# Optimization experiments

Hardware: AMD Instinct MI355X
Metric: run time of the kernel (lower is better)

Reference implementation:

```python
import jax, jax.numpy as jnp
import numpy as np

N, MEM_SIZE, MEM_DIM = 65536, 2048, 256

def setup_inputs() -> dict:
    key = jax.random.key(0)
    k1, k2 = jax.random.split(key)
    x = jax.random.normal(k1, (N, MEM_DIM), dtype=jnp.float32)
    # xavier_uniform for memory parameter [memory_size, memory_dim]
    limit = np.sqrt(6.0 / (MEM_SIZE + MEM_DIM)).astype(np.float32)
    memory = jax.random.uniform(k2, (MEM_SIZE, MEM_DIM), dtype=jnp.float32,
                                minval=-limit, maxval=limit)
    return {"x": x, "memory": memory}

def reference(x, memory):
    # scores: [N, memory_size] = x @ memory^T (unscaled)
    scores = jnp.einsum('nd,md->nm', x, memory)
    attention_weights = jax.nn.softmax(scores, axis=-1)
    memory_output = jnp.einsum('nm,md->nd', attention_weights, memory)
    return (memory_output, attention_weights)
```

## Files before the change

### kernel.cpp

```cpp
#include <hip/hip_runtime.h>
#include <hip/hip_bf16.h>
#include <stdint.h>

#define NQ 65536
#define MM 2048
#define DD 256

typedef __bf16 bf16x8 __attribute__((ext_vector_type(8)));
typedef float f32x16 __attribute__((ext_vector_type(16)));
typedef unsigned short u16;
typedef unsigned int u32;
typedef u16 u16x8 __attribute__((ext_vector_type(8)));

typedef __attribute__((address_space(3))) u32 lds_u32;
typedef __attribute__((address_space(1))) u32 glb_u32;

#define GLOAD16(gsrc, ldst)                                                    \
  __builtin_amdgcn_global_load_lds((glb_u32*)(uintptr_t)(gsrc),                \
                                   (lds_u32*)(u32)(uintptr_t)(ldst), 16, 0, 0)

__device__ __forceinline__ u16 f32_to_bf16_rtne(float v) {
  u32 u = __builtin_bit_cast(u32, v);
  u += 0x7FFFu + ((u >> 16) & 1u);
  return (u16)(u >> 16);
}

__global__ __launch_bounds__(256) void mem_convert_kernel(
    const float* __restrict__ memory, u16* __restrict__ memb,
    u16* __restrict__ memTswz) {
  int tid = blockIdx.x * 256 + threadIdx.x;
  u16 b = f32_to_bf16_rtne(memory[tid]);
  memb[tid] = b;
  int m = tid >> 8, d = tid & 255;
  int t = m >> 5, mi = m & 31;
  int c = mi >> 3, e = mi & 7;
  int slot = c ^ ((d >> 1) & 3);
  memTswz[(size_t)t * 8192 + (size_t)(d * 4 + slot) * 8 + e] = b;
}

__global__ __launch_bounds__(256, 2) void pass1_kernel(
    const float* __restrict__ x, const u16* __restrict__ memb,
    u16* __restrict__ p_e, float* __restrict__ sums) {
  __shared__ __align__(16) char stage[2][32768];

  const int tid = threadIdx.x;
  const int wv = tid >> 6;
  const int l = tid & 63;
  const int q5 = l & 31;
  const int h = l >> 5;
  const int qw = blockIdx.x * 128 + wv * 32;

  bf16x8 aq[16];
  {
    const float* xrow = x + (size_t)(qw + q5) * DD;
#pragma unroll
    for (int ks = 0; ks < 16; ++ks) {
      const float4 f0 = *(const float4*)(xrow + ks * 16 + h * 8);
      const float4 f1 = *(const float4*)(xrow + ks * 16 + h * 8 + 4);
      bf16x8 a;
      a[0] = (__bf16)f0.x; a[1] = (__bf16)f0.y;
      a[2] = (__bf16)f0.z; a[3] = (__bf16)f0.w;
      a[4] = (__bf16)f1.x; a[5] = (__bf16)f1.y;
      a[6] = (__bf16)f1.z; a[7] = (__bf16)f1.w;
      aq[ks] = a;
    }
  }

  auto STAGE1 = [&](int mt, char* buf) {
#pragma unroll
    for (int i = 0; i < 8; ++i) {
      const int wc = wv * 8 + i;
      const int row = wc * 2 + h;
      const int csrc = q5 ^ (row & 7);
      GLOAD16(memb + (((size_t)(mt * 64 + row)) << 8) + csrc * 8,
              buf + (wc << 10));
    }
  };

  float part[16];
#pragma unroll
  for (int r = 0; r < 16; ++r) part[r] = 0.f;

  STAGE1(0, stage[0]);
  __syncthreads();
  for (int mt = 0; mt < 32; ++mt) {
    char* cur = stage[mt & 1];
    char* nxt = stage[(mt & 1) ^ 1];
    if (mt + 1 < 32) STAGE1(mt + 1, nxt);
#pragma unroll
    for (int msub = 0; msub < 2; ++msub) {
      const int mrow = msub * 32 + q5;
      const char* bbase = cur + mrow * 512;
      const int sw = mrow & 7;
      f32x16 acc = 0.f;
      __builtin_amdgcn_s_setprio(1);
#pragma unroll
      for (int ks = 0; ks < 16; ++ks) {
        bf16x8 b = *(const bf16x8*)(bbase + (((ks * 2 + h) ^ sw) << 4));
        acc = __builtin_amdgcn_mfma_f32_32x32x16_bf16(aq[ks], b, acc, 0, 0, 0);
      }
      __builtin_amdgcn_s_setprio(0);
      const int tm = mt * 2 + msub;
#pragma unroll
      for (int r = 0; r < 16; ++r) {
        const int qrow = (r & 3) + 8 * (r >> 2) + 4 * h;
        const float e = __expf(acc[r]);
        part[r] += e;
        p_e[(size_t)(qw + qrow) * MM + tm * 32 + q5] = f32_to_bf16_rtne(e);
      }
    }
    __syncthreads();
  }

#pragma unroll
  for (int r = 0; r < 16; ++r) {
    float p = part[r];
    p += __shfl_xor(p, 1, 64);
    p += __shfl_xor(p, 2, 64);
    p += __shfl_xor(p, 4, 64);
    p += __shfl_xor(p, 8, 64);
    p += __shfl_xor(p, 16, 64);
    if (q5 == 0) sums[qw + (r & 3) + 8 * (r >> 2) + 4 * h] = p;
  }
}

__global__ __launch_bounds__(256, 2) void pass2_kernel(
    const u16* __restrict__ p_e, const u16* __restrict__ memTswz,
    const float* __restrict__ sums, float* __restrict__ outO,
    float* __restrict__ outW) {
  __shared__ __align__(16) char tstage[2][32768];

  const int tid = threadIdx.x;
  const int wv = tid >> 6;
  const int l = tid & 63;
  const int q5 = l & 31;
  const int h = l >> 5;
  const int qw = blockIdx.x * 128 + wv * 32;

  const float inv_lane = 1.0f / sums[qw + q5];
  float invr[16];
#pragma unroll
  for (int r = 0; r < 16; ++r) {
    invr[r] = __shfl(inv_lane, (r & 3) + 8 * (r >> 2) + 4 * h, 64);
  }

  auto STAGE2T = [&](int pr, char* buf) {
#pragma unroll
    for (int i = 0; i < 8; ++i) {
      const int ci = wv * 8 + i;
      GLOAD16(memTswz + ((size_t)pr * 2048 + ci * 64 + l) * 8,
              buf + (ci << 10));
    }
  };

  const u16* prow_base = p_e + (size_t)(qw + q5) * MM;
  u16x8 pec[4], pen[4];
#pragma unroll
  for (int j = 0; j < 4; ++j) {
    pec[j] = *(const u16x8*)(prow_base + (j >> 1) * 32 + (j & 1) * 16 + h * 8);
  }

  f32x16 oacc[8];
#pragma unroll
  for (int i = 0; i < 8; ++i) oacc[i] = 0.f;

  STAGE2T(0, tstage[0]);
  __syncthreads();
  for (int pr = 0; pr < 32; ++pr) {
    char* cur = tstage[pr & 1];
    char* nxt = tstage[(pr & 1) ^ 1];
    if (pr + 1 < 32) {
      STAGE2T(pr + 1, nxt);
      const u16* prow = prow_base + (pr + 1) * 64;
#pragma unroll
      for (int j = 0; j < 4; ++j) {
        pen[j] = *(const u16x8*)(prow + (j >> 1) * 32 + (j & 1) * 16 + h * 8);
      }
    }

#pragma unroll
    for (int tmi = 0; tmi < 2; ++tmi) {
      const char* ct = cur + tmi * 16384;
#pragma unroll
      for (int ks2 = 0; ks2 < 2; ++ks2) {
        const u16x8 pe = pec[tmi * 2 + ks2];
        float w[8];
#pragma unroll
        for (int j = 0; j < 8; ++j) {
          w[j] = __builtin_bit_cast(float, (u32)pe[j] << 16) * inv_lane;
        }
        float* base = outW + (size_t)(qw + q5) * MM + (pr * 2 + tmi) * 32 +
                      ks2 * 16 + h * 8;
        *(float4*)base = make_float4(w[0], w[1], w[2], w[3]);
        *(float4*)(base + 4) = make_float4(w[4], w[5], w[6], w[7]);
      }
      __builtin_amdgcn_s_setprio(1);
#pragma unroll
      for (int ks2 = 0; ks2 < 2; ++ks2) {
        const bf16x8 pa = __builtin_bit_cast(bf16x8, pec[tmi * 2 + ks2]);
#pragma unroll
        for (int dsub = 0; dsub < 8; ++dsub) {
          const int d = dsub * 32 + q5;
          const int slot = (2 * ks2 + h) ^ ((d >> 1) & 3);
          bf16x8 b = *(const bf16x8*)(ct + d * 64 + slot * 16);
          oacc[dsub] = __builtin_amdgcn_mfma_f32_32x32x16_bf16(pa, b,
                                                               oacc[dsub], 0,
                                                               0, 0);
        }
      }
      __builtin_amdgcn_s_setprio(0);
    }
    __syncthreads();
#pragma unroll
    for (int j = 0; j < 4; ++j) pec[j] = pen[j];
  }

#pragma unroll
  for (int dsub = 0; dsub < 8; ++dsub) {
#pragma unroll
    for (int r = 0; r < 16; ++r) {
      const int qrow = (r & 3) + 8 * (r >> 2) + 4 * h;
      outO[(size_t)(qw + qrow) * DD + dsub * 32 + q5] = oacc[dsub][r] * invr[r];
    }
  }
}

__global__ __launch_bounds__(256, 2) void pass1_fb(
    const float* __restrict__ x, const u16* __restrict__ memb,
    float* __restrict__ outWf, float* __restrict__ sums) {
  __shared__ __align__(16) char stage[2][32768];
  const int tid = threadIdx.x;
  const int wv = tid >> 6;
  const int l = tid & 63;
  const int q5 = l & 31;
  const int h = l >> 5;
  const int qw = blockIdx.x * 128 + wv * 32;

  bf16x8 aq[16];
  {
    const float* xrow = x + (size_t)(qw + q5) * DD;
#pragma unroll
    for (int ks = 0; ks < 16; ++ks) {
      const float4 f0 = *(const float4*)(xrow + ks * 16 + h * 8);
      const float4 f1 = *(const float4*)(xrow + ks * 16 + h * 8 + 4);
      bf16x8 a;
      a[0] = (__bf16)f0.x; a[1] = (__bf16)f0.y;
      a[2] = (__bf16)f0.z; a[3] = (__bf16)f0.w;
      a[4] = (__bf16)f1.x; a[5] = (__bf16)f1.y;
      a[6] = (__bf16)f1.z; a[7] = (__bf16)f1.w;
      aq[ks] = a;
    }
  }
  auto STAGE1 = [&](int mt, char* buf) {
#pragma unroll
    for (int i = 0; i < 8; ++i) {
      const int wc = wv * 8 + i;
      const int row = wc * 2 + h;
      const int csrc = q5 ^ (row & 7);
      GLOAD16(memb + (((size_t)(mt * 64 + row)) << 8) + csrc * 8,
              buf + (wc << 10));
    }
  };
  float part[16];
#pragma unroll
  for (int r = 0; r < 16; ++r) part[r] = 0.f;
  STAGE1(0, stage[0]);
  __syncthreads();
  for (int mt = 0; mt < 32; ++mt) {
    char* cur = stage[mt & 1];
    char* nxt = stage[(mt & 1) ^ 1];
    if (mt + 1 < 32) STAGE1(mt + 1, nxt);
#pragma unroll
    for (int msub = 0; msub < 2; ++msub) {
      const int mrow = msub * 32 + q5;
      const char* bbase = cur + mrow * 512;
      const int sw = mrow & 7;
      f32x16 acc = 0.f;
#pragma unroll
      for (int ks = 0; ks < 16; ++ks) {
        bf16x8 b = *(const bf16x8*)(bbase + (((ks * 2 + h) ^ sw) << 4));
        acc = __builtin_amdgcn_mfma_f32_32x32x16_bf16(aq[ks], b, acc, 0, 0, 0);
      }
      const int tm = mt * 2 + msub;
#pragma unroll
      for (int r = 0; r < 16; ++r) {
        const int qrow = (r & 3) + 8 * (r >> 2) + 4 * h;
        const float e = __expf(acc[r]);
        part[r] += e;
        outWf[(size_t)(qw + qrow) * MM + tm * 32 + q5] = e;
      }
    }
    __syncthreads();
  }
#pragma unroll
  for (int r = 0; r < 16; ++r) {
    float s = part[r];
    s += __shfl_xor(s, 1, 64);
    s += __shfl_xor(s, 2, 64);
    s += __shfl_xor(s, 4, 64);
    s += __shfl_xor(s, 8, 64);
    s += __shfl_xor(s, 16, 64);
    if (q5 == 0) sums[qw + (r & 3) + 8 * (r >> 2) + 4 * h] = s;
  }
}

__global__ __launch_bounds__(256, 2) void pass2_fb(
    const u16* __restrict__ memTswz, const float* __restrict__ sums,
    float* __restrict__ outO, float* __restrict__ outW) {
  __shared__ __align__(16) char tstage[2][16384];
  const int tid = threadIdx.x;
  const int wv = tid >> 6;
  const int l = tid & 63;
  const int q5 = l & 31;
  const int h = l >> 5;
  const int qw = blockIdx.x * 128 + wv * 32;
  const float inv_lane = 1.0f / sums[qw + q5];
  auto STAGE = [&](int t, char* buf) {
#pragma unroll
    for (int i = 0; i < 4; ++i) {
      const int ci = wv * 4 + i;
      GLOAD16(memTswz + ((size_t)t * 1024 + ci * 64 + l) * 8, buf + (ci << 10));
    }
  };
  f32x16 oacc[8];
#pragma unroll
  for (int i = 0; i < 8; ++i) oacc[i] = 0.f;
  STAGE(0, tstage[0]);
  __syncthreads();
  for (int tm = 0; tm < 64; ++tm) {
    char* cur = tstage[tm & 1];
    char* nxt = tstage[(tm & 1) ^ 1];
    if (tm + 1 < 64) STAGE(tm + 1, nxt);
    float* wrow = outW + (size_t)(qw + q5) * MM + tm * 32;
    bf16x8 pa[2];
#pragma unroll
    for (int ks2 = 0; ks2 < 2; ++ks2) {
      float4 f0 = *(const float4*)(wrow + ks2 * 16 + h * 8);
      float4 f1 = *(const float4*)(wrow + ks2 * 16 + h * 8 + 4);
      float w0 = f0.x * inv_lane, w1 = f0.y * inv_lane;
      float w2 = f0.z * inv_lane, w3 = f0.w * inv_lane;
      float w4 = f1.x * inv_lane, w5 = f1.y * inv_lane;
      float w6 = f1.z * inv_lane, w7 = f1.w * inv_lane;
      *(float4*)(wrow + ks2 * 16 + h * 8) = make_float4(w0, w1, w2, w3);
      *(float4*)(wrow + ks2 * 16 + h * 8 + 4) = make_float4(w4, w5, w6, w7);
      bf16x8 p;
      p[0] = (__bf16)w0; p[1] = (__bf16)w1; p[2] = (__bf16)w2;
      p[3] = (__bf16)w3; p[4] = (__bf16)w4; p[5] = (__bf16)w5;
      p[6] = (__bf16)w6; p[7] = (__bf16)w7;
      pa[ks2] = p;
    }
#pragma unroll
    for (int ks2 = 0; ks2 < 2; ++ks2) {
#pragma unroll
      for (int dsub = 0; dsub < 8; ++dsub) {
        const int d = dsub * 32 + q5;
        const int slot = (2 * ks2 + h) ^ ((d >> 1) & 3);
        bf16x8 b = *(const bf16x8*)(cur + d * 64 + slot * 16);
        oacc[dsub] =
            __builtin_amdgcn_mfma_f32_32x32x16_bf16(pa[ks2], b, oacc[dsub], 0,
                                                    0, 0);
      }
    }
    __syncthreads();
  }
#pragma unroll
  for (int dsub = 0; dsub < 8; ++dsub) {
#pragma unroll
    for (int r = 0; r < 16; ++r) {
      const int qrow = (r & 3) + 8 * (r >> 2) + 4 * h;
      outO[(size_t)(qw + qrow) * DD + dsub * 32 + q5] = oacc[dsub][r];
    }
  }
}

extern "C" void kernel_launch(void* const* d_in, const int* in_sizes, int n_in,
                              void* d_out, int out_size, void* d_ws,
                              size_t ws_size, hipStream_t stream) {
  const float* x = (const float*)d_in[0];
  const float* memory = (const float*)d_in[1];
  float* outO = (float*)d_out;
  float* outW = outO + (size_t)NQ * DD;

  u16* memb = (u16*)d_ws;
  u16* memTswz = memb + (size_t)MM * DD;
  float* sums = (float*)(memTswz + (size_t)MM * DD);
  u16* p_e = (u16*)(sums + NQ);
  const size_t need = (size_t)MM * DD * 2 * 2 + (size_t)NQ * 4 +
                      (size_t)NQ * MM * 2;

  mem_convert_kernel<<<dim3((MM * DD) / 256), dim3(256), 0, stream>>>(
      memory, memb, memTswz);
  if (ws_size >= need) {
    pass1_kernel<<<dim3(NQ / 128), dim3(256), 0, stream>>>(x, memb, p_e, sums);
    pass2_kernel<<<dim3(NQ / 128), dim3(256), 0, stream>>>(p_e, memTswz, sums,
                                                           outO, outW);
  } else {
    pass1_fb<<<dim3(NQ / 128), dim3(256), 0, stream>>>(x, memb, outW, sums);
    pass2_fb<<<dim3(NQ / 128), dim3(256), 0, stream>>>(memTswz, sums, outO,
                                                       outW);
  }
}
```

Before: 406.4 us.

## Fuse PV matmul into score pass and normalize weights in separate streaming kernel

Computes the exp-scores and immediately multiplies them by the memory tile (staged transposed in LDS) inside the first pass, accumulating the output in registers flash-attention style. The unnormalized output is divided by the row sums at the end. A lightweight elementwise kernel then rescales the stored bf16 exp values into the fp32 attention weights. This removes the second pass's re-read of the exp matrix for the matmul, at the cost of more registers and LDS in pass1, plus an extra wait and an LDS round-trip per tile.

```diff
diff --git a/kernel.cpp b/kernel.cpp
--- a/kernel.cpp
+++ b/kernel.cpp
@@ -40,8 +40,11 @@
 
 __global__ __launch_bounds__(256, 2) void pass1_kernel(
     const float* __restrict__ x, const u16* __restrict__ memb,
-    u16* __restrict__ p_e, float* __restrict__ sums) {
-  __shared__ __align__(16) char stage[2][32768];
+    const u16* __restrict__ memTswz, u16* __restrict__ p_e,
+    float* __restrict__ sums, float* __restrict__ outO) {
+  __shared__ __align__(16) char mb[2][16384];
+  __shared__ __align__(16) char mt[2][16384];
+  __shared__ __align__(16) u16 plds[4][32][40];
 
   const int tid = threadIdx.x;
   const int wv = tid >> 6;
@@ -66,49 +69,79 @@
     }
   }
 
-  auto STAGE1 = [&](int mt, char* buf) {
-#pragma unroll
-    for (int i = 0; i < 8; ++i) {
-      const int wc = wv * 8 + i;
+  auto STAGE_MB = [&](int t, char* buf) {
+#pragma unroll
+    for (int i = 0; i < 4; ++i) {
+      const int wc = wv * 4 + i;
       const int row = wc * 2 + h;
       const int csrc = q5 ^ (row & 7);
-      GLOAD16(memb + (((size_t)(mt * 64 + row)) << 8) + csrc * 8,
+      GLOAD16(memb + (((size_t)(t * 32 + row)) << 8) + csrc * 8,
               buf + (wc << 10));
     }
   };
+  auto STAGE_MT = [&](int t, char* buf) {
+#pragma unroll
+    for (int i = 0; i < 4; ++i) {
+      const int ci = wv * 4 + i;
+      GLOAD16(memTswz + ((size_t)t * 1024 + ci * 64 + l) * 8, buf + (ci << 10));
+    }
+  };
 
   float part[16];
 #pragma unroll
   for (int r = 0; r < 16; ++r) part[r] = 0.f;
-
-  STAGE1(0, stage[0]);
+  f32x16 oacc[8];
+#pragma unroll
+  for (int i = 0; i < 8; ++i) oacc[i] = 0.f;
+
+  STAGE_MB(0, mb[0]);
+  STAGE_MT(0, mt[0]);
   __syncthreads();
-  for (int mt = 0; mt < 32; ++mt) {
-    char* cur = stage[mt & 1];
-    char* nxt = stage[(mt & 1) ^ 1];
-    if (mt + 1 < 32) STAGE1(mt + 1, nxt);
-#pragma unroll
-    for (int msub = 0; msub < 2; ++msub) {
-      const int mrow = msub * 32 + q5;
-      const char* bbase = cur + mrow * 512;
-      const int sw = mrow & 7;
-      f32x16 acc = 0.f;
-      __builtin_amdgcn_s_setprio(1);
-#pragma unroll
-      for (int ks = 0; ks < 16; ++ks) {
-        bf16x8 b = *(const bf16x8*)(bbase + (((ks * 2 + h) ^ sw) << 4));
-        acc = __builtin_amdgcn_mfma_f32_32x32x16_bf16(aq[ks], b, acc, 0, 0, 0);
+  for (int t = 0; t < 64; ++t) {
+    const int cur = t & 1;
+    if (t + 1 < 64) {
+      STAGE_MB(t + 1, mb[cur ^ 1]);
+      STAGE_MT(t + 1, mt[cur ^ 1]);
+    }
+
+    const char* bbase = mb[cur] + q5 * 512;
+    const int sw = q5 & 7;
+    f32x16 acc = 0.f;
+    __builtin_amdgcn_s_setprio(1);
+#pragma unroll
+    for (int ks = 0; ks < 16; ++ks) {
+      bf16x8 b = *(const bf16x8*)(bbase + (((ks * 2 + h) ^ sw) << 4));
+      acc = __builtin_amdgcn_mfma_f32_32x32x16_bf16(aq[ks], b, acc, 0, 0, 0);
+    }
+    __builtin_amdgcn_s_setprio(0);
+
+#pragma unroll
+    for (int r = 0; r < 16; ++r) {
+      const int qrow = (r & 3) + 8 * (r >> 2) + 4 * h;
+      const float e = __expf(acc[r]);
+      part[r] += e;
+      const u16 eb = f32_to_bf16_rtne(e);
+      p_e[(size_t)(qw + qrow) * MM + t * 32 + q5] = eb;
+      plds[wv][qrow][q5] = eb;
+    }
+    asm volatile("s_waitcnt lgkmcnt(0)" ::: "memory");
+    __builtin_amdgcn_sched_barrier(0);
+
+    const char* ct = mt[cur];
+    __builtin_amdgcn_s_setprio(1);
+#pragma unroll
+    for (int ks2 = 0; ks2 < 2; ++ks2) {
+      const bf16x8 pa = *(const bf16x8*)&plds[wv][q5][ks2 * 16 + h * 8];
+#pragma unroll
+      for (int dsub = 0; dsub < 8; ++dsub) {
+        const int d = dsub * 32 + q5;
+        const int slot = (2 * ks2 + h) ^ ((d >> 1) & 3);
+        bf16x8 b = *(const bf16x8*)(ct + d * 64 + slot * 16);
+        oacc[dsub] =
+            __builtin_amdgcn_mfma_f32_32x32x16_bf16(pa, b, oacc[dsub], 0, 0, 0);
       }
-      __builtin_amdgcn_s_setprio(0);
-      const int tm = mt * 2 + msub;
-#pragma unroll
-      for (int r = 0; r < 16; ++r) {
-        const int qrow = (r & 3) + 8 * (r >> 2) + 4 * h;
-        const float e = __expf(acc[r]);
-        part[r] += e;
-        p_e[(size_t)(qw + qrow) * MM + tm * 32 + q5] = f32_to_bf16_rtne(e);
-      }
-    }
+    }
+    __builtin_amdgcn_s_setprio(0);
     __syncthreads();
   }
 
@@ -120,99 +153,13 @@
     p += __shfl_xor(p, 4, 64);
     p += __shfl_xor(p, 8, 64);
     p += __shfl_xor(p, 16, 64);
-    if (q5 == 0) sums[qw + (r & 3) + 8 * (r >> 2) + 4 * h] = p;
-  }
-}
-
-__global__ __launch_bounds__(256, 2) void pass2_kernel(
-    const u16* __restrict__ p_e, const u16* __restrict__ memTswz,
-    const float* __restrict__ sums, float* __restrict__ outO,
-    float* __restrict__ outW) {
-  __shared__ __align__(16) char tstage[2][32768];
-
-  const int tid = threadIdx.x;
-  const int wv = tid >> 6;
-  const int l = tid & 63;
-  const int q5 = l & 31;
-  const int h = l >> 5;
-  const int qw = blockIdx.x * 128 + wv * 32;
-
-  const float inv_lane = 1.0f / sums[qw + q5];
-  float invr[16];
-#pragma unroll
-  for (int r = 0; r < 16; ++r) {
-    invr[r] = __shfl(inv_lane, (r & 3) + 8 * (r >> 2) + 4 * h, 64);
-  }
-
-  auto STAGE2T = [&](int pr, char* buf) {
-#pragma unroll
-    for (int i = 0; i < 8; ++i) {
-      const int ci = wv * 8 + i;
-      GLOAD16(memTswz + ((size_t)pr * 2048 + ci * 64 + l) * 8,
-              buf + (ci << 10));
-    }
-  };
-
-  const u16* prow_base = p_e + (size_t)(qw + q5) * MM;
-  u16x8 pec[4], pen[4];
-#pragma unroll
-  for (int j = 0; j < 4; ++j) {
-    pec[j] = *(const u16x8*)(prow_base + (j >> 1) * 32 + (j & 1) * 16 + h * 8);
-  }
-
-  f32x16 oacc[8];
-#pragma unroll
-  for (int i = 0; i < 8; ++i) oacc[i] = 0.f;
-
-  STAGE2T(0, tstage[0]);
-  __syncthreads();
-  for (int pr = 0; pr < 32; ++pr) {
-    char* cur = tstage[pr & 1];
-    char* nxt = tstage[(pr & 1) ^ 1];
-    if (pr + 1 < 32) {
-      STAGE2T(pr + 1, nxt);
-      const u16* prow = prow_base + (pr + 1) * 64;
-#pragma unroll
-      for (int j = 0; j < 4; ++j) {
-        pen[j] = *(const u16x8*)(prow + (j >> 1) * 32 + (j & 1) * 16 + h * 8);
-      }
-    }
-
-#pragma unroll
-    for (int tmi = 0; tmi < 2; ++tmi) {
-      const char* ct = cur + tmi * 16384;
-#pragma unroll
-      for (int ks2 = 0; ks2 < 2; ++ks2) {
-        const u16x8 pe = pec[tmi * 2 + ks2];
-        float w[8];
-#pragma unroll
-        for (int j = 0; j < 8; ++j) {
-          w[j] = __builtin_bit_cast(float, (u32)pe[j] << 16) * inv_lane;
-        }
-        float* base = outW + (size_t)(qw + q5) * MM + (pr * 2 + tmi) * 32 +
-                      ks2 * 16 + h * 8;
-        *(float4*)base = make_float4(w[0], w[1], w[2], w[3]);
-        *(float4*)(base + 4) = make_float4(w[4], w[5], w[6], w[7]);
-      }
-      __builtin_amdgcn_s_setprio(1);
-#pragma unroll
-      for (int ks2 = 0; ks2 < 2; ++ks2) {
-        const bf16x8 pa = __builtin_bit_cast(bf16x8, pec[tmi * 2 + ks2]);
-#pragma unroll
-        for (int dsub = 0; dsub < 8; ++dsub) {
-          const int d = dsub * 32 + q5;
-          const int slot = (2 * ks2 + h) ^ ((d >> 1) & 3);
-          bf16x8 b = *(const bf16x8*)(ct + d * 64 + slot * 16);
-          oacc[dsub] = __builtin_amdgcn_mfma_f32_32x32x16_bf16(pa, b,
-                                                               oacc[dsub], 0,
-                                                               0, 0);
-        }
-      }
-      __builtin_amdgcn_s_setprio(0);
-    }
-    __syncthreads();
-#pragma unroll
-    for (int j = 0; j < 4; ++j) pec[j] = pen[j];
+    part[r] = p;
+  }
+  if (q5 == 0) {
+#pragma unroll
+    for (int r = 0; r < 16; ++r) {
+      sums[qw + (r & 3) + 8 * (r >> 2) + 4 * h] = part[r];
+    }
   }
 
 #pragma unroll
@@ -220,8 +167,31 @@
 #pragma unroll
     for (int r = 0; r < 16; ++r) {
       const int qrow = (r & 3) + 8 * (r >> 2) + 4 * h;
-      outO[(size_t)(qw + qrow) * DD + dsub * 32 + q5] = oacc[dsub][r] * invr[r];
-    }
+      outO[(size_t)(qw + qrow) * DD + dsub * 32 + q5] =
+          oacc[dsub][r] / part[r];
+    }
+  }
+}
+
+__global__ __launch_bounds__(256) void wnorm_kernel(
+    const u16* __restrict__ p_e, const float* __restrict__ sums,
+    float* __restrict__ outW) {
+  const int tid = blockIdx.x * 256 + threadIdx.x;
+  const int row = tid >> 6;
+  const int chunk = tid & 63;
+  const float inv = 1.0f / sums[row];
+  const u16* src = p_e + (size_t)row * MM + chunk * 32;
+  float* dst = outW + (size_t)row * MM + chunk * 32;
+#pragma unroll
+  for (int j = 0; j < 4; ++j) {
+    const u16x8 v = *(const u16x8*)(src + j * 8);
+    float w[8];
+#pragma unroll
+    for (int k = 0; k < 8; ++k) {
+      w[k] = __builtin_bit_cast(float, (u32)v[k] << 16) * inv;
+    }
+    *(float4*)(dst + j * 8) = make_float4(w[0], w[1], w[2], w[3]);
+    *(float4*)(dst + j * 8 + 4) = make_float4(w[4], w[5], w[6], w[7]);
   }
 }
 
@@ -391,9 +361,10 @@
   mem_convert_kernel<<<dim3((MM * DD) / 256), dim3(256), 0, stream>>>(
       memory, memb, memTswz);
   if (ws_size >= need) {
-    pass1_kernel<<<dim3(NQ / 128), dim3(256), 0, stream>>>(x, memb, p_e, sums);
-    pass2_kernel<<<dim3(NQ / 128), dim3(256), 0, stream>>>(p_e, memTswz, sums,
-                                                           outO, outW);
+    pass1_kernel<<<dim3(NQ / 128), dim3(256), 0, stream>>>(x, memb, memTswz,
+                                                           p_e, sums, outO);
+    wnorm_kernel<<<dim3((NQ * (MM / 32)) / 256), dim3(256), 0, stream>>>(
+        p_e, sums, outW);
   } else {
     pass1_fb<<<dim3(NQ / 128), dim3(256), 0, stream>>>(x, memb, outW, sums);
     pass2_fb<<<dim3(NQ / 128), dim3(256), 0, stream>>>(memTswz, sums, outO,
```

New measurement: 504.2 us. 1.24x slower.
